# Optimization experiments

Hardware: AMD Instinct MI355X
Metric: run time of the kernel (lower is better)

## Reference

```python
import jax, jax.numpy as jnp
import numpy as np

NUM_HEADS = 16


def sinusoidal_pe(N, C, dtype=jnp.float32):
    # matches the numpy construction in get_positional_encoding
    pos = jnp.arange(N, dtype=dtype)[:, None]                  # [N,1]
    dims = jnp.arange(C)                                        # [C]
    rates = 1.0 / jnp.power(jnp.asarray(10000.0, dtype), (2 * (dims // 2)).astype(dtype) / C)
    ang = pos * rates                                           # [N,C]
    pe = jnp.where(dims % 2 == 0, jnp.sin(ang), jnp.cos(ang))
    return pe.astype(dtype)


def setup_inputs() -> dict:
    key = jax.random.key(0)
    k1, k2, k3 = jax.random.split(key, 3)
    B, N, C = 4, 2048, 1024
    inputs = jax.random.normal(k1, (B, N, C), dtype=jnp.float32)
    mask_mat = jax.random.uniform(k2, (B, N), dtype=jnp.float32)
    # Glorot-uniform qkv kernel [C, 3C]
    limit = float(np.sqrt(6.0 / (C + 3 * C)))
    W_qkv = jax.random.uniform(k3, (C, 3 * C), dtype=jnp.float32, minval=-limit, maxval=limit)
    return {"inputs": inputs, "mask_mat": mask_mat, "W_qkv": W_qkv}


def reference(inputs, mask_mat, W_qkv):
    B, N, C = inputs.shape
    H = NUM_HEADS
    hd = C // H
    scale = hd ** (-0.5)

    # additive mask: -(m outer m), broadcast over heads
    neg_mask = -(mask_mat[:, :, None] * mask_mat[:, None, :])   # [B,N,N]

    x = inputs + sinusoidal_pe(N, C, inputs.dtype)              # APE
    qkv = jnp.einsum('bnc,cd->bnd', x, W_qkv)                   # [B,N,3C]
    qkv = qkv.reshape(B, N, 3, H, hd).transpose(2, 0, 3, 1, 4)  # [3,B,H,N,hd]
    q, k, v = qkv[0], qkv[1], qkv[2]

    attn = jnp.einsum('bhnd,bhmd->bhnm', q, k) * scale          # [B,H,N,N]
    attn = attn + neg_mask[:, None, :, :]
    attn = jax.nn.softmax(attn, axis=-1)
    out = jnp.einsum('bhnm,bhmd->bhnd', attn, v)                # [B,H,N,hd]
    return out.transpose(0, 2, 1, 3).reshape(B, N, C)
```

## Files before the change

### kernel.cpp

```cpp
#include <hip/hip_runtime.h>
#include <hip/hip_bf16.h>

typedef unsigned short u16;
typedef __bf16 bf16x8 __attribute__((ext_vector_type(8)));
typedef float floatx4 __attribute__((ext_vector_type(4)));

#define B_ 4
#define N_ 2048
#define C_ 1024
#define H_ 16
#define HD_ 64

__device__ __forceinline__ float b2f(u16 u) {
    union { float f; unsigned int i; } v; v.i = ((unsigned int)u) << 16; return v.f;
}
__device__ __forceinline__ u16 f2b(float f) {
    union { float f; unsigned int i; } v; v.f = f;
    unsigned int i = v.i;
    unsigned int r = i + 0x7FFFu + ((i >> 16) & 1u);
    return (u16)(r >> 16);
}
__device__ __forceinline__ float fexp2(float x) {
    return __builtin_amdgcn_exp2f(x);
}
__device__ __forceinline__ unsigned int pkraw(float a, float b) {
    unsigned int u;
    asm("v_cvt_pk_bf16_f32 %0, %1, %2" : "=v"(u) : "v"(a), "v"(b));
    return u;
}
__device__ __forceinline__ void async16(const u16* g, u16* l) {
    __builtin_amdgcn_global_load_lds((const __attribute__((address_space(1))) unsigned int*)g,
                                     (__attribute__((address_space(3))) unsigned int*)l,
                                     16, 0, 0);
}
__device__ __forceinline__ void async16p(const void* g, void* l) {
    __builtin_amdgcn_global_load_lds((const __attribute__((address_space(1))) unsigned int*)g,
                                     (__attribute__((address_space(3))) unsigned int*)l,
                                     16, 0, 0);
}

__global__ __launch_bounds__(256) void pe_add_kernel(const float* __restrict__ in,
                                                     u16* __restrict__ x) {
    int idx = blockIdx.x * 256 + threadIdx.x;
    int cp  = idx & 511;
    int row = idx >> 9;
    int n   = row & (N_ - 1);
    float r = exp2f(-13.287712379549449f * ((float)cp * (1.0f / 512.0f)));
    float ang = (float)n * r;
    float s, c;
    sincosf(ang, &s, &c);
    float2 pr = ((const float2*)in)[idx];
    unsigned int o = ((unsigned int)f2b(pr.y + c) << 16) | (unsigned int)f2b(pr.x + s);
    ((unsigned int*)x)[idx] = o;
}

__global__ __launch_bounds__(256) void wt_kernel(const float* __restrict__ W,
                                                 u16* __restrict__ Wt) {
    __shared__ u16 tile[32][33];
    int bx = blockIdx.x;
    int by = blockIdx.y;
    int tx = threadIdx.x & 31;
    int ty = threadIdx.x >> 5;
    for (int i = 0; i < 32; i += 8)
        tile[ty + i][tx] = f2b(W[(size_t)(by * 32 + ty + i) * 3072 + bx * 32 + tx]);
    __syncthreads();
    for (int i = 0; i < 32; i += 8)
        Wt[(size_t)(bx * 32 + ty + i) * 1024 + by * 32 + tx] = tile[tx][ty + i];
}

__global__ __launch_bounds__(256) void qkv_gemm_kernel(const u16* __restrict__ X,
                                                       const u16* __restrict__ Wt,
                                                       u16* __restrict__ q,
                                                       u16* __restrict__ k,
                                                       u16* __restrict__ vt) {
    __shared__ u16 As[128 * 64];
    __shared__ u16 Bs[128 * 64];
    int tid  = threadIdx.x;
    int wave = tid >> 6, lane = tid & 63, l15 = lane & 15, quad = lane >> 4;
    int m0 = blockIdx.x * 128;
    int n0 = blockIdx.y * 128;
    int wm = (wave & 1) * 64;
    int wn = (wave >> 1) * 64;

    floatx4 acc[4][4];
    for (int i = 0; i < 4; i++)
        for (int j = 0; j < 4; j++)
            acc[i][j] = floatx4{0.f, 0.f, 0.f, 0.f};

    int rowOff = wave * 32 + (lane >> 3);
    int colSw  = ((lane & 7) ^ (lane >> 3)) * 8;
    const u16* gA = X  + (size_t)(m0 + rowOff) * 1024 + colSw;
    const u16* gB = Wt + (size_t)(n0 + rowOff) * 1024 + colSw;
    u16* lA = As + wave * 2048;
    u16* lB = Bs + wave * 2048;

    int swl = l15 & 7;
    int aB0 = (wm + l15) * 64 + ((quad ^ swl) * 8);
    int aB1 = (wm + l15) * 64 + (((4 + quad) ^ swl) * 8);
    int bB0 = (wn + l15) * 64 + ((quad ^ swl) * 8);
    int bB1 = (wn + l15) * 64 + (((4 + quad) ^ swl) * 8);

    for (int k0 = 0; k0 < 1024; k0 += 64) {
        __syncthreads();
        async16(gA + k0,             lA);
        async16(gA + k0 +  8 * 1024, lA + 512);
        async16(gA + k0 + 16 * 1024, lA + 1024);
        async16(gA + k0 + 24 * 1024, lA + 1536);
        async16(gB + k0,             lB);
        async16(gB + k0 +  8 * 1024, lB + 512);
        async16(gB + k0 + 16 * 1024, lB + 1024);
        async16(gB + k0 + 24 * 1024, lB + 1536);
        __syncthreads();

        bf16x8 af[4][2], bf[4][2];
        for (int i = 0; i < 4; i++) {
            af[i][0] = *(const bf16x8*)(As + aB0 + i * 16 * 64);
            af[i][1] = *(const bf16x8*)(As + aB1 + i * 16 * 64);
        }
        for (int j = 0; j < 4; j++) {
            bf[j][0] = *(const bf16x8*)(Bs + bB0 + j * 16 * 64);
            bf[j][1] = *(const bf16x8*)(Bs + bB1 + j * 16 * 64);
        }
        for (int i = 0; i < 4; i++)
            for (int j = 0; j < 4; j++) {
                acc[i][j] = __builtin_amdgcn_mfma_f32_16x16x32_bf16(af[i][0], bf[j][0], acc[i][j], 0, 0, 0);
                acc[i][j] = __builtin_amdgcn_mfma_f32_16x16x32_bf16(af[i][1], bf[j][1], acc[i][j], 0, 0, 0);
            }
    }

    const float QSC = 0.125f * 1.44269504f;
    for (int i = 0; i < 4; i++) {
        int gm   = m0 + wm + i * 16 + quad * 4;
        int b    = gm >> 11;
        int nloc = gm & 2047;
        for (int j = 0; j < 4; j++) {
            int gn    = n0 + wn + j * 16 + l15;
            int which = gn >> 10;
            int cc    = gn & 1023;
            int h     = cc >> 6;
            int d     = cc & 63;
            size_t bh = (size_t)(b * 16 + h);
            if (which == 2) {
                ushort4 w4;
                w4.x = f2b(acc[i][j][0]);
                w4.y = f2b(acc[i][j][1]);
                w4.z = f2b(acc[i][j][2]);
                w4.w = f2b(acc[i][j][3]);
                *(ushort4*)(vt + (bh * 64 + d) * 2048 + nloc) = w4;
            } else {
                u16* dst = (which == 0) ? q : k;
                float sc = (which == 0) ? QSC : 1.0f;
                for (int r = 0; r < 4; r++)
                    dst[(bh * 2048 + nloc + r) * 64 + d] = f2b(acc[i][j][r] * sc);
            }
        }
    }
}

__global__ __launch_bounds__(256, 4) void attn_kernel(const u16* __restrict__ q,
                                                      const u16* __restrict__ k,
                                                      const u16* __restrict__ vt,
                                                      const float* __restrict__ mask,
                                                      float* __restrict__ out) {
    __shared__ u16 Ks[3][32 * 64];
    __shared__ u16 Vs[3][64 * 32];
    __shared__ __align__(16) float Msr[3][256];

    int tid  = threadIdx.x;
    int wave = tid >> 6, lane = tid & 63, l15 = lane & 15, quad = lane >> 4;
    int bid = blockIdx.x;
    int bh = bid & 63, qb = bid >> 6;
    int b = bh >> 4, h = bh & 15;
    size_t base = (size_t)bh * (N_ * 64);
    int q0 = qb * 128 + wave * 32;
    const float* mkb = mask + b * N_;

    bf16x8 qf[2][2];
#pragma unroll
    for (int s = 0; s < 2; s++)
#pragma unroll
        for (int dc = 0; dc < 2; dc++)
            qf[s][dc] = *(const bf16x8*)(q + base + (size_t)(q0 + s * 16 + l15) * 64 + dc * 32 + quad * 8);

    const float L2E = 1.44269504f;
    float nmq[2];
    nmq[0] = -L2E * mkb[q0 + l15];
    nmq[1] = -L2E * mkb[q0 + 16 + l15];

    bf16x8 onef;
#pragma unroll
    for (int i = 0; i < 8; i++) onef[i] = (__bf16)1.0f;

    floatx4 acc[2][4];
    floatx4 accl[2];
#pragma unroll
    for (int s = 0; s < 2; s++) {
        accl[s] = floatx4{0.f, 0.f, 0.f, 0.f};
#pragma unroll
        for (int dt = 0; dt < 4; dt++)
            acc[s][dt] = floatx4{0.f, 0.f, 0.f, 0.f};
    }

    int krow = wave * 8  + (lane >> 3);
    int kcol = ((lane & 7) ^ (lane >> 3)) * 8;
    int vrow = wave * 16 + (lane >> 2);
    int vcol = ((lane & 3) ^ ((lane >> 2) & 3) ^ ((lane >> 4) & 3)) * 8;
    const u16* gK = k  + base + (size_t)krow * 64 + kcol;
    const u16* gV = vt + ((size_t)bh * 64 + vrow) * 2048 + vcol;
    const float* gM = mkb + (lane & 7) * 4;
    int wof = wave * 512;

    int a0 = ((quad    ) ^ (l15 & 7)) * 8;
    int a1 = ((4 + quad) ^ (l15 & 7)) * 8;
    int vsw = (l15 & 3) ^ ((l15 >> 2) & 3);
    int o1 = (((quad >> 1)    ) ^ vsw) * 8 + (quad & 1) * 4;
    int o2 = (((quad >> 1) + 2) ^ vsw) * 8 + (quad & 1) * 4;

    auto TILE = [&](int kt, const u16* Kb, const u16* Vb, const float* Mb,
                    u16* Kn, u16* Vn, float* Mn) {
        asm volatile("s_waitcnt vmcnt(3)" ::: "memory");
        __builtin_amdgcn_s_barrier();
        __builtin_amdgcn_sched_barrier(0);
        int nkt = kt + 64; if (nkt > N_ - 32) nkt = N_ - 32;
        async16(gK + (size_t)nkt * 64, Kn);
        async16(gV + nkt,              Vn);
        async16p(gM + nkt,             Mn);
        float4 mkv0 = *(const float4*)(Mb + quad * 4);
        float4 mkv1 = *(const float4*)(Mb + 16 + quad * 4);
        float p[2][2][4];
#pragma unroll
        for (int t = 0; t < 2; t++) {
            bf16x8 kf0 = *(const bf16x8*)(Kb + (t * 16 + l15) * 64 + a0);
            bf16x8 kf1 = *(const bf16x8*)(Kb + (t * 16 + l15) * 64 + a1);
            float4 mk = t ? mkv1 : mkv0;
#pragma unroll
            for (int s = 0; s < 2; s++) {
                floatx4 sa;
                sa[0] = nmq[s] * mk.x;
                sa[1] = nmq[s] * mk.y;
                sa[2] = nmq[s] * mk.z;
                sa[3] = nmq[s] * mk.w;
                __builtin_amdgcn_s_setprio(1);
                sa = __builtin_amdgcn_mfma_f32_16x16x32_bf16(kf0, qf[s][0], sa, 0, 0, 0);
                sa = __builtin_amdgcn_mfma_f32_16x16x32_bf16(kf1, qf[s][1], sa, 0, 0, 0);
                __builtin_amdgcn_s_setprio(0);
                p[s][t][0] = fexp2(sa[0]);
                p[s][t][1] = fexp2(sa[1]);
                p[s][t][2] = fexp2(sa[2]);
                p[s][t][3] = fexp2(sa[3]);
            }
        }
        bf16x8 pf[2];
#pragma unroll
        for (int s = 0; s < 2; s++) {
            uint4 u;
            u.x = pkraw(p[s][0][0], p[s][0][1]);
            u.y = pkraw(p[s][0][2], p[s][0][3]);
            u.z = pkraw(p[s][1][0], p[s][1][1]);
            u.w = pkraw(p[s][1][2], p[s][1][3]);
            __builtin_memcpy(&pf[s], &u, 16);
        }
        __builtin_amdgcn_s_setprio(1);
        accl[0] = __builtin_amdgcn_mfma_f32_16x16x32_bf16(pf[0], onef, accl[0], 0, 0, 0);
        accl[1] = __builtin_amdgcn_mfma_f32_16x16x32_bf16(pf[1], onef, accl[1], 0, 0, 0);
        __builtin_amdgcn_s_setprio(0);
#pragma unroll
        for (int dt = 0; dt < 4; dt++) {
            const u16* vr = Vb + (dt * 16 + l15) * 32;
            uint2 v1 = *(const uint2*)(vr + o1);
            uint2 v2 = *(const uint2*)(vr + o2);
            uint4 vv; vv.x = v1.x; vv.y = v1.y; vv.z = v2.x; vv.w = v2.y;
            bf16x8 vf; __builtin_memcpy(&vf, &vv, 16);
            __builtin_amdgcn_s_setprio(1);
            acc[0][dt] = __builtin_amdgcn_mfma_f32_16x16x32_bf16(pf[0], vf, acc[0][dt], 0, 0, 0);
            acc[1][dt] = __builtin_amdgcn_mfma_f32_16x16x32_bf16(pf[1], vf, acc[1][dt], 0, 0, 0);
            __builtin_amdgcn_s_setprio(0);
        }
    };

    asm volatile("s_waitcnt vmcnt(0)" ::: "memory");
    async16(gK,            Ks[0] + wof);
    async16(gV,            Vs[0] + wof);
    async16p(gM,           Msr[0]);
    async16(gK + 32 * 64,  Ks[1] + wof);
    async16(gV + 32,       Vs[1] + wof);
    async16p(gM + 32,      Msr[1]);
    __syncthreads();

    for (int m = 0; m < 21; ++m) {
        int kt = m * 96;
        TILE(kt,      Ks[0], Vs[0], Msr[0], Ks[2] + wof, Vs[2] + wof, Msr[2]);
        TILE(kt + 32, Ks[1], Vs[1], Msr[1], Ks[0] + wof, Vs[0] + wof, Msr[0]);
        TILE(kt + 64, Ks[2], Vs[2], Msr[2], Ks[1] + wof, Vs[1] + wof, Msr[1]);
    }
    TILE(2016, Ks[0], Vs[0], Msr[0], Ks[2] + wof, Vs[2] + wof, Msr[2]);

#pragma unroll
    for (int s = 0; s < 2; s++) {
#pragma unroll
        for (int r = 0; r < 4; r++) {
            float ir = 1.0f / accl[s][r];
            int qrow = q0 + s * 16 + quad * 4 + r;
            float* orow = out + ((size_t)(b * N_ + qrow)) * C_ + h * 64;
#pragma unroll
            for (int dt = 0; dt < 4; dt++)
                orow[dt * 16 + l15] = acc[s][dt][r] * ir;
        }
    }
}

extern "C" void kernel_launch(void* const* d_in, const int* in_sizes, int n_in,
                              void* d_out, int out_size, void* d_ws, size_t ws_size,
                              hipStream_t stream) {
    const float* inp  = (const float*)d_in[0];
    const float* mask = (const float*)d_in[1];
    const float* W    = (const float*)d_in[2];
    float* out = (float*)d_out;

    char* ws = (char*)d_ws;
    u16* x  = (u16*)ws;
    u16* Wt = (u16*)(ws + 16777216);
    u16* q  = (u16*)(ws + 23068672);
    u16* k  = q + 8388608;
    u16* vt = k + 8388608;

    pe_add_kernel<<<16384, 256, 0, stream>>>(inp, x);
    wt_kernel<<<dim3(96, 32), 256, 0, stream>>>(W, Wt);
    qkv_gemm_kernel<<<dim3(64, 24), 256, 0, stream>>>(x, Wt, q, k, vt);
    attn_kernel<<<1024, 256, 0, stream>>>(q, k, vt, mask, out);
}
```

Baseline: 230.8 us.

## Double-buffer QKV GEMM LDS tiles with async prefetch; use fast sin/cos in PE

The QKV projection GEMM now uses two LDS buffers per operand and issues the async global-to-LDS loads for the next K tile before computing on the current one. It relies on vmcnt waits and raw barriers in place of the previous two __syncthreads per iteration. The aim is to hide global load latency behind MFMA work, at the cost of doubling LDS use (which may lower occupancy) and issuing one redundant final load. The positional-encoding kernel also switches to hardware exp2 and the __sinf/__cosf intrinsics, which are less accurate for large angles.

New measurement: 229.9 us. No clear change (-0.4%).

```diff
diff --git a/kernel.cpp b/kernel.cpp
--- a/kernel.cpp
+++ b/kernel.cpp
@@ -45,10 +45,10 @@
     int cp  = idx & 511;
     int row = idx >> 9;
     int n   = row & (N_ - 1);
-    float r = exp2f(-13.287712379549449f * ((float)cp * (1.0f / 512.0f)));
+    float r = fexp2(-13.287712379549449f * ((float)cp * (1.0f / 512.0f)));
     float ang = (float)n * r;
-    float s, c;
-    sincosf(ang, &s, &c);
+    float s = __sinf(ang);
+    float c = __cosf(ang);
     float2 pr = ((const float2*)in)[idx];
     unsigned int o = ((unsigned int)f2b(pr.y + c) << 16) | (unsigned int)f2b(pr.x + s);
     ((unsigned int*)x)[idx] = o;
@@ -73,8 +73,10 @@
                                                        u16* __restrict__ q,
                                                        u16* __restrict__ k,
                                                        u16* __restrict__ vt) {
-    __shared__ u16 As[128 * 64];
-    __shared__ u16 Bs[128 * 64];
+    __shared__ u16 As0[128 * 64];
+    __shared__ u16 As1[128 * 64];
+    __shared__ u16 Bs0[128 * 64];
+    __shared__ u16 Bs1[128 * 64];
     int tid  = threadIdx.x;
     int wave = tid >> 6, lane = tid & 63, l15 = lane & 15, quad = lane >> 4;
     int m0 = blockIdx.x * 128;
@@ -91,8 +93,7 @@
     int colSw  = ((lane & 7) ^ (lane >> 3)) * 8;
     const u16* gA = X  + (size_t)(m0 + rowOff) * 1024 + colSw;
     const u16* gB = Wt + (size_t)(n0 + rowOff) * 1024 + colSw;
-    u16* lA = As + wave * 2048;
-    u16* lB = Bs + wave * 2048;
+    int wof = wave * 2048;
 
     int swl = l15 & 7;
     int aB0 = (wm + l15) * 64 + ((quad ^ swl) * 8);
@@ -100,32 +101,52 @@
     int bB0 = (wn + l15) * 64 + ((quad ^ swl) * 8);
     int bB1 = (wn + l15) * 64 + (((4 + quad) ^ swl) * 8);
 
-    for (int k0 = 0; k0 < 1024; k0 += 64) {
-        __syncthreads();
-        async16(gA + k0,             lA);
-        async16(gA + k0 +  8 * 1024, lA + 512);
-        async16(gA + k0 + 16 * 1024, lA + 1024);
-        async16(gA + k0 + 24 * 1024, lA + 1536);
-        async16(gB + k0,             lB);
-        async16(gB + k0 +  8 * 1024, lB + 512);
-        async16(gB + k0 + 16 * 1024, lB + 1024);
-        async16(gB + k0 + 24 * 1024, lB + 1536);
-        __syncthreads();
-
+    auto STAGE = [&](int k0, u16* A, u16* B) {
+        async16(gA + k0,             A + wof);
+        async16(gA + k0 +  8 * 1024, A + wof + 512);
+        async16(gA + k0 + 16 * 1024, A + wof + 1024);
+        async16(gA + k0 + 24 * 1024, A + wof + 1536);
+        async16(gB + k0,             B + wof);
+        async16(gB + k0 +  8 * 1024, B + wof + 512);
+        async16(gB + k0 + 16 * 1024, B + wof + 1024);
+        async16(gB + k0 + 24 * 1024, B + wof + 1536);
+    };
+    auto COMPUTE = [&](const u16* A, const u16* B) {
         bf16x8 af[4][2], bf[4][2];
+#pragma unroll
         for (int i = 0; i < 4; i++) {
-            af[i][0] = *(const bf16x8*)(As + aB0 + i * 16 * 64);
-            af[i][1] = *(const bf16x8*)(As + aB1 + i * 16 * 64);
-        }
+            af[i][0] = *(const bf16x8*)(A + aB0 + i * 1024);
+            af[i][1] = *(const bf16x8*)(A + aB1 + i * 1024);
+        }
+#pragma unroll
         for (int j = 0; j < 4; j++) {
-            bf[j][0] = *(const bf16x8*)(Bs + bB0 + j * 16 * 64);
-            bf[j][1] = *(const bf16x8*)(Bs + bB1 + j * 16 * 64);
-        }
+            bf[j][0] = *(const bf16x8*)(B + bB0 + j * 1024);
+            bf[j][1] = *(const bf16x8*)(B + bB1 + j * 1024);
+        }
+#pragma unroll
         for (int i = 0; i < 4; i++)
+#pragma unroll
             for (int j = 0; j < 4; j++) {
                 acc[i][j] = __builtin_amdgcn_mfma_f32_16x16x32_bf16(af[i][0], bf[j][0], acc[i][j], 0, 0, 0);
                 acc[i][j] = __builtin_amdgcn_mfma_f32_16x16x32_bf16(af[i][1], bf[j][1], acc[i][j], 0, 0, 0);
             }
+    };
+
+    STAGE(0, As0, Bs0);
+    for (int t = 0; t < 16; t += 2) {
+        STAGE((t + 1) * 64, As1, Bs1);
+        asm volatile("s_waitcnt vmcnt(8)" ::: "memory");
+        __builtin_amdgcn_s_barrier();
+        __builtin_amdgcn_sched_barrier(0);
+        COMPUTE(As0, Bs0);
+        __builtin_amdgcn_s_barrier();
+        int k2 = (t + 2 < 16) ? (t + 2) * 64 : 960;
+        STAGE(k2, As0, Bs0);
+        asm volatile("s_waitcnt vmcnt(8)" ::: "memory");
+        __builtin_amdgcn_s_barrier();
+        __builtin_amdgcn_sched_barrier(0);
+        COMPUTE(As1, Bs1);
+        __builtin_amdgcn_s_barrier();
     }
 
     const float QSC = 0.125f * 1.44269504f;
```
